# Kernel tuning notes

Hardware: AMD Instinct MI355X
Metric: run time of the kernel (lower is better)

The kernel has to match this reference:

```python
import jax, jax.numpy as jnp
import numpy as np

DIM = 192
HEADS = 6
HEAD_DIM = DIM // HEADS
WS = 8
SHIFT = WS // 2
B, H, W = 32, 64, 64
EPS = 1e-5


def _rel_pos_index(ws):
    coords = np.stack(np.meshgrid(np.arange(ws), np.arange(ws), indexing='ij'))  # [2,ws,ws]
    cf = coords.reshape(2, -1)  # [2,N]
    rel = cf[:, :, None] - cf[:, None, :]  # [2,N,N]
    rel = rel.transpose(1, 2, 0)
    rel[:, :, 0] += ws - 1
    rel[:, :, 1] += ws - 1
    rel[:, :, 0] *= 2 * ws - 1
    return jnp.asarray(rel.sum(-1))  # [N,N] int32


def _shift_mask(Hp, Wp, ws, shift):
    img = np.zeros((Hp, Wp))
    slices = (slice(0, -ws), slice(-ws, -shift), slice(-shift, None))
    cnt = 0
    for hs in slices:
        for wsl in slices:
            img[hs, wsl] = cnt
            cnt += 1
    m = img.reshape(Hp // ws, ws, Wp // ws, ws).transpose(0, 2, 1, 3).reshape(-1, ws * ws)
    diff = m[:, None, :] - m[:, :, None]
    return jnp.asarray(np.where(diff != 0, -100.0, 0.0).astype(np.float32))  # [nW,N,N]


def _layernorm(x, g, b):
    mu = x.mean(-1, keepdims=True)
    var = ((x - mu) ** 2).mean(-1, keepdims=True)
    return (x - mu) / jnp.sqrt(var + EPS) * g + b


def _win_part(x, ws):
    b, h, w, c = x.shape
    x = x.reshape(b, h // ws, ws, w // ws, ws, c).transpose(0, 1, 3, 2, 4, 5)
    return x.reshape(-1, ws * ws, c)


def _win_rev(win, ws, h, w):
    b = win.shape[0] // (h * w // ws // ws)
    x = win.reshape(b, h // ws, w // ws, ws, ws, -1).transpose(0, 1, 3, 2, 4, 5)
    return x.reshape(b, h, w, -1)


def setup_inputs() -> dict:
    key = jax.random.key(0)
    ks = jax.random.split(key, 6)
    d = DIM
    init = lambda k, shape, scale: jax.random.normal(k, shape, jnp.float32) * scale
    return {
        'x': jax.random.normal(ks[0], (B, H, W, d), jnp.float32),
        'ln1_g': jnp.ones((d,), jnp.float32),
        'ln1_b': jnp.zeros((d,), jnp.float32),
        'qkv_w': init(ks[1], (3 * d, d), 0.02),
        'qkv_b': jnp.zeros((3 * d,), jnp.float32),
        'proj_w': init(ks[2], (d, d), 0.02),
        'proj_b': jnp.zeros((d,), jnp.float32),
        'rel_bias_table': init(ks[3], ((2 * WS - 1) ** 2, HEADS), 0.02),
        'ln2_g': jnp.ones((d,), jnp.float32),
        'ln2_b': jnp.zeros((d,), jnp.float32),
        'mlp_w1': init(ks[4], (4 * d, d), 0.02),
        'mlp_b1': jnp.zeros((4 * d,), jnp.float32),
        'mlp_w2': init(ks[5], (d, 4 * d), 0.02),
        'mlp_b2': jnp.zeros((d,), jnp.float32),
    }


def reference(x, ln1_g, ln1_b, qkv_w, qkv_b, proj_w, proj_b, rel_bias_table, ln2_g, ln2_b, mlp_w1, mlp_b1, mlp_w2, mlp_b2):
    b, h, w, c = x.shape
    N = WS * WS
    shortcut = x
    y = _layernorm(x, ln1_g, ln1_b)
    # shifted window: roll, partition
    y = jnp.roll(y, shift=(-SHIFT, -SHIFT), axis=(1, 2))
    xw = _win_part(y, WS)  # [B_, N, C]
    B_ = xw.shape[0]
    qkv = (xw @ qkv_w.T + qkv_b).reshape(B_, N, 3, HEADS, HEAD_DIM)
    q, k, v = qkv[:, :, 0], qkv[:, :, 1], qkv[:, :, 2]  # [B_, N, H, hd]
    scale = HEAD_DIM ** -0.5
    attn = jnp.einsum('bnhd,bmhd->bhnm', q * scale, k)  # [B_, H, N, N]
    rel = rel_bias_table[_rel_pos_index(WS)]  # [N, N, heads]
    attn = attn + rel.transpose(2, 0, 1)[None]
    mask = _shift_mask(h, w, WS, SHIFT)  # [nW, N, N]
    nW = mask.shape[0]
    attn = attn.reshape(B_ // nW, nW, HEADS, N, N) + mask[None, :, None]
    attn = jax.nn.softmax(attn.reshape(B_, HEADS, N, N), axis=-1)
    out = jnp.einsum('bhnm,bmhd->bnhd', attn, v).reshape(B_, N, c)
    out = out @ proj_w.T + proj_b
    y = _win_rev(out, WS, h, w)
    y = jnp.roll(y, shift=(SHIFT, SHIFT), axis=(1, 2))
    x2 = shortcut + y
    z = _layernorm(x2, ln2_g, ln2_b)
    z = jax.nn.gelu(z @ mlp_w1.T + mlp_b1, approximate=False) @ mlp_w2.T + mlp_b2
    return x2 + z
```

## Files before the change

kernel.cpp:

```cpp
#include <hip/hip_runtime.h>
#include <hip/hip_bf16.h>

typedef __bf16 bf16_t;
typedef __bf16 bf16x8 __attribute__((ext_vector_type(8)));
typedef float f32x4 __attribute__((ext_vector_type(4)));

#define MFMA16x16(a, b, c) __builtin_amdgcn_mfma_f32_16x16x32_bf16((a), (b), (c), 0, 0, 0)

constexpr int DIM = 192;
constexpr int NHEAD = 6;
constexpr int NWIN = 2048;
constexpr int WTOK = 64;


__global__ __launch_bounds__(256) void cvt_qkvwf(const float* __restrict__ s, bf16_t* __restrict__ d) {
    const int t = blockIdx.x * 256 + threadIdx.x;
    if (t >= 216 * 64) return;
    const int lane = t & 63, f = t >> 6;
    const int nt = f & 1, kk = (f >> 1) % 6, ph = f / 12;
    const int row = ph * 32 + nt * 16 + (lane & 15);
    const int col = kk * 32 + (lane >> 4) * 8;
    const float* sp = s + row * 192 + col;
    bf16_t* dp = d + (size_t)t * 8;
#pragma unroll
    for (int e = 0; e < 8; ++e) dp[e] = (bf16_t)sp[e];
}

__global__ __launch_bounds__(256) void cvt_projwf(const float* __restrict__ s, bf16_t* __restrict__ d) {
    const int t = blockIdx.x * 256 + threadIdx.x;
    if (t >= 72 * 64) return;
    const int lane = t & 63, f = t >> 6;
    const int nt = f % 3, kk = (f / 3) % 6, wv = f / 18;
    const int row = wv * 48 + nt * 16 + (lane & 15);
    const int col = kk * 32 + (lane >> 4) * 8;
    const float* sp = s + row * 192 + col;
    bf16_t* dp = d + (size_t)t * 8;
#pragma unroll
    for (int e = 0; e < 8; ++e) dp[e] = (bf16_t)sp[e];
}

__global__ __launch_bounds__(256) void cvt_w1f(const float* __restrict__ s, bf16_t* __restrict__ d) {
    const int t = blockIdx.x * 256 + threadIdx.x;
    if (t >= 288 * 64) return;
    const int lane = t & 63, f = t >> 6;
    const int nt = f % 3, kk = (f / 3) % 6, q = f / 18;
    const int wv = q & 3, kc = q >> 2;
    const int row = kc * 192 + wv * 48 + nt * 16 + (lane & 15);
    const int col = kk * 32 + (lane >> 4) * 8;
    const float* sp = s + row * 192 + col;
    bf16_t* dp = d + (size_t)t * 8;
#pragma unroll
    for (int e = 0; e < 8; ++e) dp[e] = (bf16_t)sp[e];
}

__global__ __launch_bounds__(256) void cvt_w2f(const float* __restrict__ s, bf16_t* __restrict__ d) {
    const int t = blockIdx.x * 256 + threadIdx.x;
    if (t >= 288 * 64) return;
    const int lane = t & 63, f = t >> 6;
    const int nt = f % 3, kk = (f / 3) % 6, q = f / 18;
    const int wv = q & 3, kc = q >> 2;
    const int row = wv * 48 + nt * 16 + (lane & 15);
    const int col = kc * 192 + kk * 32 + (lane >> 4) * 8;
    const float* sp = s + row * 768 + col;
    bf16_t* dp = d + (size_t)t * 8;
#pragma unroll
    for (int e = 0; e < 8; ++e) dp[e] = (bf16_t)sp[e];
}

__global__ __launch_bounds__(256) void ln_win_kernel(const float* __restrict__ in,
                                                     const float* __restrict__ g,
                                                     const float* __restrict__ bta,
                                                     bf16_t* __restrict__ ywf) {
    __shared__ bf16_t y_s[64][200];
    const int tid = threadIdx.x, lane = tid & 63, wv = tid >> 6;
    const int win = blockIdx.x;
    const int b_ = win >> 6, hb = (win >> 3) & 7, wb = win & 7;
    const float gv0 = g[lane], gv1 = g[lane + 64], gv2 = g[lane + 128];
    const float bv0 = bta[lane], bv1 = bta[lane + 64], bv2 = bta[lane + 128];
    for (int i = 0; i < 16; ++i) {
        const int n = wv * 16 + i;
        const int th = n >> 3, tw = n & 7;
        const int hh = (hb * 8 + th + 4) & 63;
        const int ww = (wb * 8 + tw + 4) & 63;
        const size_t src = ((size_t)(b_ * 64 + hh) * 64 + ww) * DIM;
        const float v0 = in[src + lane], v1 = in[src + lane + 64], v2 = in[src + lane + 128];
        float sm = v0 + v1 + v2;
        float q = v0 * v0 + v1 * v1 + v2 * v2;
#pragma unroll
        for (int m = 1; m < 64; m <<= 1) {
            sm += __shfl_xor(sm, m);
            q += __shfl_xor(q, m);
        }
        const float mu = sm * (1.0f / DIM);
        const float inv = rsqrtf(q * (1.0f / DIM) - mu * mu + 1e-5f);
        y_s[n][lane]       = (bf16_t)((v0 - mu) * inv * gv0 + bv0);
        y_s[n][lane + 64]  = (bf16_t)((v1 - mu) * inv * gv1 + bv1);
        y_s[n][lane + 128] = (bf16_t)((v2 - mu) * inv * gv2 + bv2);
    }
    __syncthreads();
    bf16_t* dst = ywf + (size_t)win * 12288;
    for (int j = tid; j < 1536; j += 256) {
        const int f = j >> 6, ln = j & 63;
        const int mt = f & 3, kk = f >> 2;
        const int row = mt * 16 + (ln & 15), col = kk * 32 + (ln >> 4) * 8;
        *reinterpret_cast<bf16x8*>(dst + (size_t)j * 8) =
            *reinterpret_cast<const bf16x8*>(&y_s[row][col]);
    }
}

__global__ __launch_bounds__(256) void ln2_kernel(const float* __restrict__ in,
                                                  const float* __restrict__ g,
                                                  const float* __restrict__ bta,
                                                  bf16_t* __restrict__ out) {
    const int wid = blockIdx.x * 4 + (threadIdx.x >> 6);
    const int lane = threadIdx.x & 63;
    const size_t src = (size_t)wid * DIM;
    const float v0 = in[src + lane];
    const float v1 = in[src + lane + 64];
    const float v2 = in[src + lane + 128];
    float s = v0 + v1 + v2;
    float q = v0 * v0 + v1 * v1 + v2 * v2;
#pragma unroll
    for (int m = 1; m < 64; m <<= 1) {
        s += __shfl_xor(s, m);
        q += __shfl_xor(q, m);
    }
    const float mu = s * (1.0f / DIM);
    const float var = q * (1.0f / DIM) - mu * mu;
    const float inv = rsqrtf(var + 1e-5f);
    out[src + lane]       = (bf16_t)((v0 - mu) * inv * g[lane] + bta[lane]);
    out[src + lane + 64]  = (bf16_t)((v1 - mu) * inv * g[lane + 64] + bta[lane + 64]);
    out[src + lane + 128] = (bf16_t)((v2 - mu) * inv * g[lane + 128] + bta[lane + 128]);
}

__global__ __launch_bounds__(64, 3) void attn_kernel(const bf16_t* __restrict__ ywf,
                                                     const bf16_t* __restrict__ qkvwf,
                                                     const float* __restrict__ qkvb,
                                                     const float* __restrict__ relb,
                                                     bf16_t* __restrict__ aout) {
    __shared__ bf16_t scr[6400];
    const int lane = threadIdx.x;
    const int l15 = lane & 15, l4 = lane >> 4;
    const int wh = (blockIdx.x & 7) * ((NWIN * NHEAD) >> 3) + (blockIdx.x >> 3);
    const int win = wh / 6;
    const int h = wh - win * 6;
    const bf16_t* ywin = ywf + (size_t)win * 12288;

    bf16_t* tb = scr;
    bf16_t* vtb = scr + 4096;

    auto part_gemm = [&](int ph, f32x4 (&acc)[4][2]) {
#pragma unroll
        for (int kk = 0; kk < 6; ++kk) {
            bf16x8 a[4], b[2];
#pragma unroll
            for (int mt = 0; mt < 4; ++mt)
                a[mt] = *reinterpret_cast<const bf16x8*>(ywin + ((kk * 4 + mt) << 9) + lane * 8);
#pragma unroll
            for (int nt = 0; nt < 2; ++nt)
                b[nt] = *reinterpret_cast<const bf16x8*>(
                    qkvwf + (size_t)((((ph * 6 + kk) << 1) + nt) << 9) + lane * 8);
#pragma unroll
            for (int mt = 0; mt < 4; ++mt)
#pragma unroll
                for (int nt = 0; nt < 2; ++nt)
                    acc[mt][nt] = MFMA16x16(a[mt], b[nt], acc[mt][nt]);
        }
    };

    {
        f32x4 acc[4][2] = {};
        const int ph = 12 + h;
        part_gemm(ph, acc);
#pragma unroll
        for (int nt = 0; nt < 2; ++nt) {
            const int d = nt * 16 + l15;
            const float bias = qkvb[ph * 32 + d];
#pragma unroll
            for (int mt = 0; mt < 4; ++mt)
#pragma unroll
                for (int r = 0; r < 4; ++r)
                    vtb[d * 72 + mt * 16 + l4 * 4 + r] = (bf16_t)(acc[mt][nt][r] + bias);
        }
    }
    {
        f32x4 acc[4][2] = {};
        const int ph = h;
        part_gemm(ph, acc);
#pragma unroll
        for (int nt = 0; nt < 2; ++nt) {
            const int d = nt * 16 + l15;
            const float bias = qkvb[ph * 32 + d];
#pragma unroll
            for (int mt = 0; mt < 4; ++mt)
#pragma unroll
                for (int r = 0; r < 4; ++r)
                    tb[(mt * 16 + l4 * 4 + r) * 40 + d] =
                        (bf16_t)((acc[mt][nt][r] + bias) * 0.17677669529663689f);
        }
    }
    bf16x8 aq[4];
#pragma unroll
    for (int mt = 0; mt < 4; ++mt)
        aq[mt] = *reinterpret_cast<const bf16x8*>(&tb[(mt * 16 + l15) * 40 + l4 * 8]);

    {
        f32x4 acc[4][2] = {};
        const int ph = 6 + h;
        part_gemm(ph, acc);
#pragma unroll
        for (int nt = 0; nt < 2; ++nt) {
            const int d = nt * 16 + l15;
            const float bias = qkvb[ph * 32 + d];
#pragma unroll
            for (int mt = 0; mt < 4; ++mt)
#pragma unroll
                for (int r = 0; r < 4; ++r)
                    tb[(mt * 16 + l4 * 4 + r) * 40 + d] = (bf16_t)(acc[mt][nt][r] + bias);
        }
    }
    bf16x8 bk[4];
#pragma unroll
    for (int nt = 0; nt < 4; ++nt)
        bk[nt] = *reinterpret_cast<const bf16x8*>(&tb[(nt * 16 + l15) * 40 + l4 * 8]);

    f32x4 s[4][4] = {};
#pragma unroll
    for (int mt = 0; mt < 4; ++mt)
#pragma unroll
        for (int nt = 0; nt < 4; ++nt)
            s[mt][nt] = MFMA16x16(aq[mt], bk[nt], s[mt][nt]);

    const int hb = (win >> 3) & 7, wb = win & 7;
    int colc[4], colreg[4];
#pragma unroll
    for (int nt = 0; nt < 4; ++nt) {
        const int m = nt * 16 + l15;
        const int mh = m >> 3, mw = m & 7;
        colc[nt] = mh * 15 + mw;
        const int gh = hb * 8 + mh, gw = wb * 8 + mw;
        const int rh = (gh < 56) ? 0 : ((gh < 60) ? 1 : 2);
        const int rw = (gw < 56) ? 0 : ((gw < 60) ? 1 : 2);
        colreg[nt] = rh * 3 + rw;
    }
#pragma unroll
    for (int mt = 0; mt < 4; ++mt) {
#pragma unroll
        for (int r = 0; r < 4; ++r) {
            const int n = mt * 16 + l4 * 4 + r;
            const int nh = n >> 3, nw = n & 7;
            const int rowc = nh * 15 + nw + 112;
            const int gh = hb * 8 + nh, gw = wb * 8 + nw;
            const int rh = (gh < 56) ? 0 : ((gh < 60) ? 1 : 2);
            const int rw = (gw < 56) ? 0 : ((gw < 60) ? 1 : 2);
            const int rreg = rh * 3 + rw;
            float vals[4];
            float mx = -1e30f;
#pragma unroll
            for (int nt = 0; nt < 4; ++nt) {
                float v = s[mt][nt][r] + relb[(rowc - colc[nt]) * NHEAD + h];
                if (rreg != colreg[nt]) v -= 100.0f;
                vals[nt] = v;
                mx = fmaxf(mx, v);
            }
            mx = fmaxf(mx, __shfl_xor(mx, 1));
            mx = fmaxf(mx, __shfl_xor(mx, 2));
            mx = fmaxf(mx, __shfl_xor(mx, 4));
            mx = fmaxf(mx, __shfl_xor(mx, 8));
            float sum = 0.f;
#pragma unroll
            for (int nt = 0; nt < 4; ++nt) {
                vals[nt] = __expf(vals[nt] - mx);
                sum += vals[nt];
            }
            sum += __shfl_xor(sum, 1);
            sum += __shfl_xor(sum, 2);
            sum += __shfl_xor(sum, 4);
            sum += __shfl_xor(sum, 8);
            const float inv = 1.0f / sum;
            const int nsw = n & 7;
#pragma unroll
            for (int nt = 0; nt < 4; ++nt) {
                const int tk = nt * 16 + l15;
                tb[n * 64 + (((tk >> 3) ^ nsw) << 3) + (tk & 7)] = (bf16_t)(vals[nt] * inv);
            }
        }
    }

    f32x4 o[4][2] = {};
#pragma unroll
    for (int kk = 0; kk < 2; ++kk) {
        bf16x8 a[4], b[2];
#pragma unroll
        for (int mt = 0; mt < 4; ++mt) {
            const int tq = mt * 16 + l15;
            a[mt] = *reinterpret_cast<const bf16x8*>(&tb[tq * 64 + (((kk * 4 + l4) ^ (tq & 7)) << 3)]);
        }
#pragma unroll
        for (int nt = 0; nt < 2; ++nt)
            b[nt] = *reinterpret_cast<const bf16x8*>(&vtb[(nt * 16 + l15) * 72 + kk * 32 + l4 * 8]);
#pragma unroll
        for (int mt = 0; mt < 4; ++mt)
#pragma unroll
            for (int nt = 0; nt < 2; ++nt)
                o[mt][nt] = MFMA16x16(a[mt], b[nt], o[mt][nt]);
    }
    bf16_t* op = aout + (size_t)win * (WTOK * DIM) + h * 32;
#pragma unroll
    for (int mt = 0; mt < 4; ++mt)
#pragma unroll
        for (int nt = 0; nt < 2; ++nt)
#pragma unroll
            for (int r = 0; r < 4; ++r) {
                const int n = mt * 16 + l4 * 4 + r;
                op[n * DIM + nt * 16 + l15] = (bf16_t)o[mt][nt][r];
            }
}

__global__ __launch_bounds__(256) void proj_kernel(const bf16_t* __restrict__ ain,
                                                   const bf16_t* __restrict__ pwf,
                                                   const float* __restrict__ pbias,
                                                   const float* __restrict__ x,
                                                   float* __restrict__ x2) {
    __shared__ bf16_t a_s[64][200];
    const int tid = threadIdx.x;
    const int lane = tid & 63;
    const int wv = tid >> 6;
    const int win = blockIdx.x;
    const int l15 = lane & 15, l4 = lane >> 4;

    const bf16_t* asrc = ain + (size_t)win * (WTOK * DIM);
    for (int i = tid; i < WTOK * DIM / 8; i += 256) {
        const int idx = i * 8;
        *reinterpret_cast<bf16x8*>(&a_s[idx / DIM][idx % DIM]) =
            *reinterpret_cast<const bf16x8*>(asrc + idx);
    }
    __syncthreads();

    const int n0 = wv * 48;
    f32x4 acc[4][3] = {};
    for (int kk = 0; kk < 6; ++kk) {
        const int c0 = kk * 32 + l4 * 8;
        bf16x8 a[4], b[3];
#pragma unroll
        for (int mt = 0; mt < 4; ++mt)
            a[mt] = *reinterpret_cast<const bf16x8*>(&a_s[mt * 16 + l15][c0]);
#pragma unroll
        for (int nt = 0; nt < 3; ++nt)
            b[nt] = *reinterpret_cast<const bf16x8*>(
                pwf + (size_t)(((wv * 6 + kk) * 3 + nt) << 9) + lane * 8);
#pragma unroll
        for (int mt = 0; mt < 4; ++mt)
#pragma unroll
            for (int nt = 0; nt < 3; ++nt)
                acc[mt][nt] = MFMA16x16(a[mt], b[nt], acc[mt][nt]);
    }
    const int b_ = win >> 6, hb = (win >> 3) & 7, wb = win & 7;
#pragma unroll
    for (int mt = 0; mt < 4; ++mt)
#pragma unroll
        for (int r = 0; r < 4; ++r) {
            const int n = mt * 16 + l4 * 4 + r;
            const int th = n >> 3, tw = n & 7;
            const int hh = (hb * 8 + th + 4) & 63;
            const int ww = (wb * 8 + tw + 4) & 63;
            const size_t row = ((size_t)(b_ * 64 + hh) * 64 + ww) * DIM;
#pragma unroll
            for (int nt = 0; nt < 3; ++nt) {
                const int col = n0 + nt * 16 + l15;
                x2[row + col] = acc[mt][nt][r] + pbias[col] + x[row + col];
            }
        }
}

__device__ __forceinline__ float gelu_f(float v) {
    const float ax = fabsf(v) * 0.70710678118654752f;
    const float t = __builtin_amdgcn_rcpf(1.0f + 0.3275911f * ax);
    float p = 1.061405429f;
    p = p * t - 1.453152027f;
    p = p * t + 1.421413741f;
    p = p * t - 0.284496736f;
    p = p * t + 0.254829592f;
    p = p * t;
    const float e = 1.0f - p * __expf(-ax * ax);
    return 0.5f * v * (1.0f + copysignf(e, v));
}

__global__ __launch_bounds__(256, 3) void mlp_kernel(const bf16_t* __restrict__ z,
                                                     const bf16_t* __restrict__ w1f,
                                                     const float* __restrict__ b1,
                                                     const bf16_t* __restrict__ w2f,
                                                     const float* __restrict__ b2,
                                                     float* __restrict__ xout) {
    __shared__ bf16_t z_s[64][200];
    __shared__ bf16_t h_s[64][200];
    const int tid = threadIdx.x, lane = tid & 63, wv = tid >> 6;
    const int l15 = lane & 15, l4 = lane >> 4;
    const size_t t0 = (size_t)blockIdx.x * 64;
    const int n0 = wv * 48;

    const bf16_t* zsrc = z + t0 * DIM;
    for (int i = tid; i < WTOK * DIM / 8; i += 256) {
        const int idx = i * 8;
        *reinterpret_cast<bf16x8*>(&z_s[idx / DIM][idx % DIM]) =
            *reinterpret_cast<const bf16x8*>(zsrc + idx);
    }
    __syncthreads();

    f32x4 acc_o[4][3] = {};
    for (int kc = 0; kc < 4; ++kc) {
        const int fb = (kc * 4 + wv) * 18;
        f32x4 hacc[4][3] = {};
#pragma unroll
        for (int kk = 0; kk < 6; ++kk) {
            const int c0 = kk * 32 + l4 * 8;
            bf16x8 a[4], b[3];
#pragma unroll
            for (int mt = 0; mt < 4; ++mt)
                a[mt] = *reinterpret_cast<const bf16x8*>(&z_s[mt * 16 + l15][c0]);
#pragma unroll
            for (int nt = 0; nt < 3; ++nt)
                b[nt] = *reinterpret_cast<const bf16x8*>(
                    w1f + (size_t)((fb + kk * 3 + nt) << 9) + lane * 8);
#pragma unroll
            for (int mt = 0; mt < 4; ++mt)
#pragma unroll
                for (int nt = 0; nt < 3; ++nt)
                    hacc[mt][nt] = MFMA16x16(a[mt], b[nt], hacc[mt][nt]);
        }
        __syncthreads();
#pragma unroll
        for (int mt = 0; mt < 4; ++mt)
#pragma unroll
            for (int r = 0; r < 4; ++r) {
                const int n = mt * 16 + l4 * 4 + r;
#pragma unroll
                for (int nt = 0; nt < 3; ++nt) {
                    const int col = n0 + nt * 16 + l15;
                    h_s[n][col] = (bf16_t)gelu_f(hacc[mt][nt][r] + b1[kc * 192 + col]);
                }
            }
        __syncthreads();
#pragma unroll
        for (int kk = 0; kk < 6; ++kk) {
            const int c0 = kk * 32 + l4 * 8;
            bf16x8 a[4], b[3];
#pragma unroll
            for (int mt = 0; mt < 4; ++mt)
                a[mt] = *reinterpret_cast<const bf16x8*>(&h_s[mt * 16 + l15][c0]);
#pragma unroll
            for (int nt = 0; nt < 3; ++nt)
                b[nt] = *reinterpret_cast<const bf16x8*>(
                    w2f + (size_t)((fb + kk * 3 + nt) << 9) + lane * 8);
#pragma unroll
            for (int mt = 0; mt < 4; ++mt)
#pragma unroll
                for (int nt = 0; nt < 3; ++nt)
                    acc_o[mt][nt] = MFMA16x16(a[mt], b[nt], acc_o[mt][nt]);
        }
    }
#pragma unroll
    for (int mt = 0; mt < 4; ++mt)
#pragma unroll
        for (int r = 0; r < 4; ++r) {
            const int n = mt * 16 + l4 * 4 + r;
            const size_t addr = (t0 + n) * DIM;
#pragma unroll
            for (int nt = 0; nt < 3; ++nt) {
                const int col = n0 + nt * 16 + l15;
                xout[addr + col] = acc_o[mt][nt][r] + b2[col] + xout[addr + col];
            }
        }
}

extern "C" void kernel_launch(void* const* d_in, const int* in_sizes, int n_in,
                              void* d_out, int out_size, void* d_ws, size_t ws_size,
                              hipStream_t stream) {
    const float* x      = (const float*)d_in[0];
    const float* ln1_g  = (const float*)d_in[1];
    const float* ln1_b  = (const float*)d_in[2];
    const float* qkv_w  = (const float*)d_in[3];
    const float* qkv_b  = (const float*)d_in[4];
    const float* proj_w = (const float*)d_in[5];
    const float* proj_b = (const float*)d_in[6];
    const float* relb   = (const float*)d_in[7];
    const float* ln2_g  = (const float*)d_in[8];
    const float* ln2_b  = (const float*)d_in[9];
    const float* mlp_w1 = (const float*)d_in[10];
    const float* mlp_b1 = (const float*)d_in[11];
    const float* mlp_w2 = (const float*)d_in[12];
    const float* mlp_b2 = (const float*)d_in[13];
    float* out = (float*)d_out;

    char* ws = (char*)d_ws;
    bf16_t* qkvwf = (bf16_t*)(ws + 0);
    bf16_t* pwf   = (bf16_t*)(ws + 221184);
    bf16_t* w1f   = (bf16_t*)(ws + 294912);
    bf16_t* w2f   = (bf16_t*)(ws + 589824);
    bf16_t* bufA  = (bf16_t*)(ws + 884736);
    bf16_t* bufB  = (bf16_t*)(ws + 884736 + 50331648);

    cvt_qkvwf<<<54, 256, 0, stream>>>(qkv_w, qkvwf);
    cvt_projwf<<<18, 256, 0, stream>>>(proj_w, pwf);
    cvt_w1f<<<72, 256, 0, stream>>>(mlp_w1, w1f);
    cvt_w2f<<<72, 256, 0, stream>>>(mlp_w2, w2f);

    ln_win_kernel<<<NWIN, 256, 0, stream>>>(x, ln1_g, ln1_b, bufA);
    attn_kernel<<<NWIN * NHEAD, 64, 0, stream>>>(bufA, qkvwf, qkv_b, relb, bufB);
    proj_kernel<<<NWIN, 256, 0, stream>>>(bufB, pwf, proj_b, x, out);
    ln2_kernel<<<32768, 256, 0, stream>>>(out, ln2_g, ln2_b, bufA);
    mlp_kernel<<<2048, 256, 0, stream>>>(bufA, w1f, mlp_b1, w2f, mlp_b2, out);
}
```

Before: 362.7 us.

## Emit LN2 output in MFMA fragment layout and drop MLP z staging

LN2 now normalizes 64 tokens per block and writes the bf16 result pre-swizzled into MFMA A-fragment order. The MLP kernel reads A fragments directly from global memory instead of staging z in shared memory. This frees one LDS buffer, so occupancy is raised to 4 blocks per CU. GELU is switched from the erf polynomial to a cheaper tanh-style sigmoid form, which changes numerics slightly relative to exact erf GELU.

```diff
diff --git a/kernel.cpp b/kernel.cpp
--- a/kernel.cpp
+++ b/kernel.cpp
@@ -108,29 +108,41 @@
     }
 }
 
-__global__ __launch_bounds__(256) void ln2_kernel(const float* __restrict__ in,
-                                                  const float* __restrict__ g,
-                                                  const float* __restrict__ bta,
-                                                  bf16_t* __restrict__ out) {
-    const int wid = blockIdx.x * 4 + (threadIdx.x >> 6);
-    const int lane = threadIdx.x & 63;
-    const size_t src = (size_t)wid * DIM;
-    const float v0 = in[src + lane];
-    const float v1 = in[src + lane + 64];
-    const float v2 = in[src + lane + 128];
-    float s = v0 + v1 + v2;
-    float q = v0 * v0 + v1 * v1 + v2 * v2;
-#pragma unroll
-    for (int m = 1; m < 64; m <<= 1) {
-        s += __shfl_xor(s, m);
-        q += __shfl_xor(q, m);
-    }
-    const float mu = s * (1.0f / DIM);
-    const float var = q * (1.0f / DIM) - mu * mu;
-    const float inv = rsqrtf(var + 1e-5f);
-    out[src + lane]       = (bf16_t)((v0 - mu) * inv * g[lane] + bta[lane]);
-    out[src + lane + 64]  = (bf16_t)((v1 - mu) * inv * g[lane + 64] + bta[lane + 64]);
-    out[src + lane + 128] = (bf16_t)((v2 - mu) * inv * g[lane + 128] + bta[lane + 128]);
+__global__ __launch_bounds__(256) void ln2f_kernel(const float* __restrict__ in,
+                                                   const float* __restrict__ g,
+                                                   const float* __restrict__ bta,
+                                                   bf16_t* __restrict__ zf) {
+    __shared__ bf16_t y_s[64][200];
+    const int tid = threadIdx.x, lane = tid & 63, wv = tid >> 6;
+    const size_t t0 = (size_t)blockIdx.x * 64;
+    const float gv0 = g[lane], gv1 = g[lane + 64], gv2 = g[lane + 128];
+    const float bv0 = bta[lane], bv1 = bta[lane + 64], bv2 = bta[lane + 128];
+    for (int i = 0; i < 16; ++i) {
+        const int n = wv * 16 + i;
+        const size_t src = (t0 + n) * DIM;
+        const float v0 = in[src + lane], v1 = in[src + lane + 64], v2 = in[src + lane + 128];
+        float sm = v0 + v1 + v2;
+        float q = v0 * v0 + v1 * v1 + v2 * v2;
+#pragma unroll
+        for (int m = 1; m < 64; m <<= 1) {
+            sm += __shfl_xor(sm, m);
+            q += __shfl_xor(q, m);
+        }
+        const float mu = sm * (1.0f / DIM);
+        const float inv = rsqrtf(q * (1.0f / DIM) - mu * mu + 1e-5f);
+        y_s[n][lane]       = (bf16_t)((v0 - mu) * inv * gv0 + bv0);
+        y_s[n][lane + 64]  = (bf16_t)((v1 - mu) * inv * gv1 + bv1);
+        y_s[n][lane + 128] = (bf16_t)((v2 - mu) * inv * gv2 + bv2);
+    }
+    __syncthreads();
+    bf16_t* dst = zf + (size_t)blockIdx.x * 12288;
+    for (int j = tid; j < 1536; j += 256) {
+        const int f = j >> 6, ln = j & 63;
+        const int mt = f & 3, kk = f >> 2;
+        const int row = mt * 16 + (ln & 15), col = kk * 32 + (ln >> 4) * 8;
+        *reinterpret_cast<bf16x8*>(dst + (size_t)j * 8) =
+            *reinterpret_cast<const bf16x8*>(&y_s[row][col]);
+    }
 }
 
 __global__ __launch_bounds__(64, 3) void attn_kernel(const bf16_t* __restrict__ ywf,
@@ -374,38 +386,25 @@
 }
 
 __device__ __forceinline__ float gelu_f(float v) {
-    const float ax = fabsf(v) * 0.70710678118654752f;
-    const float t = __builtin_amdgcn_rcpf(1.0f + 0.3275911f * ax);
-    float p = 1.061405429f;
-    p = p * t - 1.453152027f;
-    p = p * t + 1.421413741f;
-    p = p * t - 0.284496736f;
-    p = p * t + 0.254829592f;
-    p = p * t;
-    const float e = 1.0f - p * __expf(-ax * ax);
-    return 0.5f * v * (1.0f + copysignf(e, v));
-}
-
-__global__ __launch_bounds__(256, 3) void mlp_kernel(const bf16_t* __restrict__ z,
+    const float x2 = v * v;
+    const float inner = fmaf(0.044715f * x2, v, v);
+    const float e = __expf(inner * 1.5957691216057308f);
+    const float r = __builtin_amdgcn_rcpf(e + 1.0f);
+    return v - v * r;
+}
+
+__global__ __launch_bounds__(256, 4) void mlp_kernel(const bf16_t* __restrict__ zf,
                                                      const bf16_t* __restrict__ w1f,
                                                      const float* __restrict__ b1,
                                                      const bf16_t* __restrict__ w2f,
                                                      const float* __restrict__ b2,
                                                      float* __restrict__ xout) {
-    __shared__ bf16_t z_s[64][200];
     __shared__ bf16_t h_s[64][200];
     const int tid = threadIdx.x, lane = tid & 63, wv = tid >> 6;
     const int l15 = lane & 15, l4 = lane >> 4;
     const size_t t0 = (size_t)blockIdx.x * 64;
     const int n0 = wv * 48;
-
-    const bf16_t* zsrc = z + t0 * DIM;
-    for (int i = tid; i < WTOK * DIM / 8; i += 256) {
-        const int idx = i * 8;
-        *reinterpret_cast<bf16x8*>(&z_s[idx / DIM][idx % DIM]) =
-            *reinterpret_cast<const bf16x8*>(zsrc + idx);
-    }
-    __syncthreads();
+    const bf16_t* ztile = zf + (size_t)blockIdx.x * 12288;
 
     f32x4 acc_o[4][3] = {};
     for (int kc = 0; kc < 4; ++kc) {
@@ -413,11 +412,10 @@
         f32x4 hacc[4][3] = {};
 #pragma unroll
         for (int kk = 0; kk < 6; ++kk) {
-            const int c0 = kk * 32 + l4 * 8;
             bf16x8 a[4], b[3];
 #pragma unroll
             for (int mt = 0; mt < 4; ++mt)
-                a[mt] = *reinterpret_cast<const bf16x8*>(&z_s[mt * 16 + l15][c0]);
+                a[mt] = *reinterpret_cast<const bf16x8*>(ztile + ((kk * 4 + mt) << 9) + lane * 8);
 #pragma unroll
             for (int nt = 0; nt < 3; ++nt)
                 b[nt] = *reinterpret_cast<const bf16x8*>(
@@ -508,6 +506,6 @@
     ln_win_kernel<<<NWIN, 256, 0, stream>>>(x, ln1_g, ln1_b, bufA);
     attn_kernel<<<NWIN * NHEAD, 64, 0, stream>>>(bufA, qkvwf, qkv_b, relb, bufB);
     proj_kernel<<<NWIN, 256, 0, stream>>>(bufB, pwf, proj_b, x, out);
-    ln2_kernel<<<32768, 256, 0, stream>>>(out, ln2_g, ln2_b, bufA);
+    ln2f_kernel<<<2048, 256, 0, stream>>>(out, ln2_g, ln2_b, bufA);
     mlp_kernel<<<2048, 256, 0, stream>>>(bufA, w1f, mlp_b1, w2f, mlp_b2, out);
 }
```

Result: slower. 519.3 us (+43.2%).
